# Kernel tuning notes

Hardware: AMD Instinct MI355X
Metric: run time of the kernel (lower is better)

Reference implementation:

```python
import jax, jax.numpy as jnp
import numpy as np

N = 50000
E = 800000
D = 128
LN_EPS = 1e-5


def setup_inputs() -> dict:
    key = jax.random.key(0)
    k1, k2, k3, k4 = jax.random.split(key, 4)
    x = jax.random.normal(k1, (N, D), dtype=jnp.float32)
    edge_index = jax.random.randint(k2, (2, E), 0, N, dtype=jnp.int32)
    # xavier_uniform with gain=sqrt(2) (relu gain)
    gain = float(np.sqrt(2.0))
    lim_lin = gain * float(np.sqrt(6.0 / (D + D)))
    W_lin = jax.random.uniform(k3, (D, D), dtype=jnp.float32, minval=-lim_lin, maxval=lim_lin)
    lim_attn = gain * float(np.sqrt(6.0 / (2 * D + 1)))
    W_attn = jax.random.uniform(k4, (1, 2 * D), dtype=jnp.float32, minval=-lim_attn, maxval=lim_attn)
    ln_scale = jnp.ones((D,), dtype=jnp.float32)
    ln_bias = jnp.zeros((D,), dtype=jnp.float32)
    return {"x": x, "W_lin": W_lin, "W_attn": W_attn,
            "ln_scale": ln_scale, "ln_bias": ln_bias, "edge_index": edge_index}


def _layer_norm(h, scale, bias):
    mu = jnp.mean(h, axis=-1, keepdims=True)
    var = jnp.mean(jnp.square(h - mu), axis=-1, keepdims=True)
    return (h - mu) * jax.lax.rsqrt(var + LN_EPS) * scale + bias


def reference(x, W_lin, W_attn, ln_scale, ln_bias, edge_index):
    n = x.shape[0]
    src, dst = edge_index[0], edge_index[1]
    # h = x @ W_lin^T  [N, D]
    h = jnp.einsum('nd,od->no', x, W_lin)
    # attention score: [h_src || h_dst] @ W_attn^T == h_src@a_src + h_dst@a_dst
    d = h.shape[1]
    a_src = W_attn[0, :d]
    a_dst = W_attn[0, d:]
    s_src = h @ a_src  # [N]
    s_dst = h @ a_dst  # [N]
    scores = s_src[src] + s_dst[dst]  # [E]
    scores = jnp.where(scores >= 0, scores, 0.2 * scores)  # leaky_relu(0.2)
    # segment softmax over edges grouped by dst
    seg_max = jax.ops.segment_max(scores, dst, num_segments=n)  # [N]
    seg_max = jnp.where(jnp.isfinite(seg_max), seg_max, 0.0)
    ex = jnp.exp(scores - seg_max[dst])  # [E]
    denom = jax.ops.segment_sum(ex, dst, num_segments=n)  # [N]
    alpha = ex / jnp.where(denom > 0, denom, 1.0)[dst]  # [E]
    # weighted message aggregation (dropout is identity in eval mode)
    msgs = h[src] * alpha[:, None]  # [E, D]
    agg = jax.ops.segment_sum(msgs, dst, num_segments=n)  # [N, D]
    # residual (input_dim == output_dim -> no projection) + layer norm
    return _layer_norm(agg + x, ln_scale, ln_bias)
```

## Files before the change

kernel.cpp:

```cpp
#include <hip/hip_runtime.h>

#define N_NODES 50000
#define E_EDGES 800000
#define D_DIM   128
#define LN_EPS  1e-5f
#define SCAN_BLOCKS 196
#define HIST_BLOCKS 3125
#define GEMM_BLOCKS 391

typedef __bf16 bf16x8 __attribute__((ext_vector_type(8)));
typedef unsigned short ushort8v __attribute__((ext_vector_type(8)));
typedef float f32x4 __attribute__((ext_vector_type(4)));
typedef int i32x2v __attribute__((ext_vector_type(2)));
typedef int i32x16v __attribute__((ext_vector_type(16)));

__device__ inline unsigned short f2b(float f) {
    unsigned int u = __float_as_uint(f);
    unsigned int r = u + 0x7FFFu + ((u >> 16) & 1u);
    return (unsigned short)(r >> 16);
}
__device__ inline float b2f(unsigned short h) {
    return __uint_as_float((unsigned int)h << 16);
}
__device__ inline float blo(unsigned int u) { return __uint_as_float(u << 16); }
__device__ inline float bhi(unsigned int u) { return __uint_as_float(u & 0xFFFF0000u); }

__device__ inline i32x16v sload16(const uint2* p) {
    i32x16v r;
    asm volatile("s_load_dwordx16 %0, %1, 0x0\n\ts_waitcnt lgkmcnt(0)"
                 : "=&s"(r) : "s"(p));
    return r;
}
__device__ inline i32x2v sload2(const uint2* p) {
    i32x2v r;
    asm volatile("s_load_dwordx2 %0, %1, 0x0\n\ts_waitcnt lgkmcnt(0)"
                 : "=&s"(r) : "s"(p));
    return r;
}

__global__ void k_prep(const float* __restrict__ W,
                       unsigned short* __restrict__ Whp,
                       unsigned short* __restrict__ Wlp,
                       int* __restrict__ count) {
    int i = blockIdx.x * 256 + threadIdx.x;
    if (i < N_NODES) count[i] = 0;
    if (i < 16384) {
        int o = i >> 7, k = i & 127;
        float v = W[i];
        unsigned short h = f2b(v);
        unsigned short l = f2b(v - b2f(h));
        int idx = (k >> 3) * 1024 + o * 8 + (k & 7);
        Whp[idx] = h;
        Wlp[idx] = l;
    }
}

__global__ __launch_bounds__(256, 2) void k_gemm_hist(
        const float* __restrict__ x, const unsigned short* __restrict__ Wpk,
        const float* __restrict__ Wa, const int* __restrict__ dst,
        int* __restrict__ count, unsigned short* __restrict__ hb,
        float* __restrict__ ssrc, float* __restrict__ sdst) {
    __shared__ float4 wl4[4096];
    const int tid = threadIdx.x;

    if (blockIdx.x >= GEMM_BLOCKS) {
        int e = (blockIdx.x - GEMM_BLOCKS) * 256 + tid;
        atomicAdd(&count[dst[e]], 1);
        return;
    }

    {
        const float4* wsrc = (const float4*)Wpk;
        #pragma unroll
        for (int i = 0; i < 16; ++i)
            wl4[i * 256 + tid] = wsrc[i * 256 + tid];
    }

    const int c = tid & 15;
    const int g = (tid >> 4) & 3;
    const int w = tid >> 6;
    const int n0 = blockIdx.x * 128;

    bf16x8 ah[2][4], al[2][4];
    #pragma unroll
    for (int t = 0; t < 2; ++t) {
        int n = n0 + w * 32 + t * 16 + c;
        if (n > N_NODES - 1) n = N_NODES - 1;
        const float* xr = x + (size_t)n * 128;
        #pragma unroll
        for (int s = 0; s < 4; ++s) {
            float4 f0 = *(const float4*)(xr + s * 32 + g * 8);
            float4 f1 = *(const float4*)(xr + s * 32 + g * 8 + 4);
            float fv[8] = {f0.x, f0.y, f0.z, f0.w, f1.x, f1.y, f1.z, f1.w};
            ushort8v uh, ul;
            #pragma unroll
            for (int j = 0; j < 8; ++j) {
                unsigned short hj = f2b(fv[j]);
                uh[j] = hj;
                ul[j] = f2b(fv[j] - b2f(hj));
            }
            ah[t][s] = __builtin_bit_cast(bf16x8, uh);
            al[t][s] = __builtin_bit_cast(bf16x8, ul);
        }
    }

    __syncthreads();
    const bf16x8* wb = (const bf16x8*)wl4;

    f32x4 acc[2][8];
    #pragma unroll
    for (int t = 0; t < 2; ++t)
        #pragma unroll
        for (int cb = 0; cb < 8; ++cb)
            acc[t][cb] = (f32x4){0.f, 0.f, 0.f, 0.f};

    #pragma unroll
    for (int cb = 0; cb < 8; ++cb) {
        #pragma unroll
        for (int s = 0; s < 4; ++s) {
            int q = (s * 4 + g) * 128 + cb * 16 + c;
            bf16x8 bh = wb[q];
            bf16x8 bl = wb[2048 + q];
            acc[0][cb] = __builtin_amdgcn_mfma_f32_16x16x32_bf16(ah[0][s], bh, acc[0][cb], 0, 0, 0);
            acc[1][cb] = __builtin_amdgcn_mfma_f32_16x16x32_bf16(ah[1][s], bh, acc[1][cb], 0, 0, 0);
            acc[0][cb] = __builtin_amdgcn_mfma_f32_16x16x32_bf16(al[0][s], bh, acc[0][cb], 0, 0, 0);
            acc[1][cb] = __builtin_amdgcn_mfma_f32_16x16x32_bf16(al[1][s], bh, acc[1][cb], 0, 0, 0);
            acc[0][cb] = __builtin_amdgcn_mfma_f32_16x16x32_bf16(ah[0][s], bl, acc[0][cb], 0, 0, 0);
            acc[1][cb] = __builtin_amdgcn_mfma_f32_16x16x32_bf16(ah[1][s], bl, acc[1][cb], 0, 0, 0);
        }
    }

    float asv[8], adv[8];
    #pragma unroll
    for (int cb = 0; cb < 8; ++cb) {
        asv[cb] = Wa[cb * 16 + c];
        adv[cb] = Wa[128 + cb * 16 + c];
    }
    #pragma unroll
    for (int t = 0; t < 2; ++t) {
        #pragma unroll
        for (int i = 0; i < 4; ++i) {
            int n = n0 + w * 32 + t * 16 + g * 4 + i;
            float ps = 0.f, pd = 0.f;
            #pragma unroll
            for (int cb = 0; cb < 8; ++cb) {
                float v = acc[t][cb][i];
                ps += v * asv[cb];
                pd += v * adv[cb];
            }
            #pragma unroll
            for (int off = 1; off < 16; off <<= 1) {
                ps += __shfl_xor(ps, off);
                pd += __shfl_xor(pd, off);
            }
            if (n < N_NODES) {
                size_t rb = (size_t)n * 128 + c;
                #pragma unroll
                for (int cb = 0; cb < 8; ++cb)
                    hb[rb + cb * 16] = f2b(acc[t][cb][i]);
                if (c == 0) { ssrc[n] = ps; sdst[n] = pd; }
            }
        }
    }
}

__global__ __launch_bounds__(256) void k_scan1(const int* __restrict__ count,
                                               int* __restrict__ rowptr,
                                               int* __restrict__ bsum) {
    __shared__ int wsum[4];
    const int tid  = threadIdx.x;
    const int lane = tid & 63, w = tid >> 6;
    int i = blockIdx.x * 256 + tid;
    int v = (i < N_NODES) ? count[i] : 0;
    int sc = v;
    #pragma unroll
    for (int off = 1; off < 64; off <<= 1) {
        int t = __shfl_up(sc, off);
        if (lane >= off) sc += t;
    }
    if (lane == 63) wsum[w] = sc;
    __syncthreads();
    if (tid == 0) {
        int s0 = wsum[0], s1 = wsum[1], s2 = wsum[2], s3 = wsum[3];
        wsum[0] = 0; wsum[1] = s0; wsum[2] = s0 + s1; wsum[3] = s0 + s1 + s2;
        bsum[blockIdx.x] = s0 + s1 + s2 + s3;
    }
    __syncthreads();
    if (i < N_NODES) rowptr[i] = sc - v + wsum[w];
}

__global__ __launch_bounds__(256) void k_scan2(int* __restrict__ bsum) {
    __shared__ int wsum[4];
    const int tid  = threadIdx.x;
    const int lane = tid & 63, w = tid >> 6;
    int v = (tid < SCAN_BLOCKS) ? bsum[tid] : 0;
    int sc = v;
    #pragma unroll
    for (int off = 1; off < 64; off <<= 1) {
        int t = __shfl_up(sc, off);
        if (lane >= off) sc += t;
    }
    if (lane == 63) wsum[w] = sc;
    __syncthreads();
    if (tid == 0) {
        int s0 = wsum[0], s1 = wsum[1], s2 = wsum[2];
        wsum[3] = s0 + s1 + s2; wsum[2] = s0 + s1; wsum[1] = s0; wsum[0] = 0;
    }
    __syncthreads();
    if (tid < SCAN_BLOCKS) bsum[tid] = sc - v + wsum[w];
}

__global__ void k_scatter(const int* __restrict__ src, const int* __restrict__ dst,
                          const float* __restrict__ ssrc, const float* __restrict__ sdst,
                          const int* __restrict__ rowptr, const int* __restrict__ bsum,
                          int* __restrict__ count, uint2* __restrict__ sev) {
    int e = blockIdx.x * 256 + threadIdx.x;
    int s  = src[e];
    int dv = dst[e];
    float sc = ssrc[s] + sdst[dv];
    sc = sc >= 0.f ? sc : 0.2f * sc;
    float ex = __expf(sc);
    int pos = rowptr[dv] + bsum[dv >> 8] + (atomicSub(&count[dv], 1) - 1);
    sev[pos] = make_uint2((unsigned int)s, __float_as_uint(ex));
}

__global__ __launch_bounds__(256) void k_gather(
        const int* __restrict__ rowptr, const int* __restrict__ bsum,
        const uint2* __restrict__ sev,
        const unsigned short* __restrict__ hb, const float* __restrict__ x,
        const float* __restrict__ scale, const float* __restrict__ bias,
        float* __restrict__ out) {
    int n    = __builtin_amdgcn_readfirstlane(blockIdx.x * 4 + (threadIdx.x >> 6));
    int lane = threadIdx.x & 63;
    int beg = rowptr[n] + bsum[n >> 8];
    int end = (n == N_NODES - 1) ? E_EDGES : rowptr[n + 1] + bsum[(n + 1) >> 8];
    const unsigned int* hb32 = (const unsigned int*)hb;

    float a0 = 0.f, a1 = 0.f, b0 = 0.f, b1 = 0.f, den = 0.f, den2 = 0.f;

    int i = beg;
    for (; i + 15 < end; i += 16) {
        int ib = __builtin_amdgcn_readfirstlane(i);
        i32x16v s0 = sload16(sev + ib);
        i32x16v s1 = sload16(sev + ib + 8);
        unsigned int u[16];
        #pragma unroll
        for (int q = 0; q < 8; ++q)
            u[q] = hb32[(((unsigned)s0[2 * q]) << 6) + lane];
        #pragma unroll
        for (int q = 0; q < 8; ++q)
            u[8 + q] = hb32[(((unsigned)s1[2 * q]) << 6) + lane];
        #pragma unroll
        for (int q = 0; q < 8; q += 2) {
            float ex0 = __uint_as_float(s0[2 * q + 1]);
            float ex1 = __uint_as_float(s0[2 * q + 3]);
            den  += ex0; den2 += ex1;
            a0 += ex0 * blo(u[q]);     a1 += ex0 * bhi(u[q]);
            b0 += ex1 * blo(u[q + 1]); b1 += ex1 * bhi(u[q + 1]);
        }
        #pragma unroll
        for (int q = 0; q < 8; q += 2) {
            float ex0 = __uint_as_float(s1[2 * q + 1]);
            float ex1 = __uint_as_float(s1[2 * q + 3]);
            den  += ex0; den2 += ex1;
            a0 += ex0 * blo(u[8 + q]);     a1 += ex0 * bhi(u[8 + q]);
            b0 += ex1 * blo(u[8 + q + 1]); b1 += ex1 * bhi(u[8 + q + 1]);
        }
    }
    for (; i + 7 < end; i += 8) {
        int ib = __builtin_amdgcn_readfirstlane(i);
        i32x16v s0 = sload16(sev + ib);
        unsigned int u[8];
        #pragma unroll
        for (int q = 0; q < 8; ++q)
            u[q] = hb32[(((unsigned)s0[2 * q]) << 6) + lane];
        #pragma unroll
        for (int q = 0; q < 8; q += 2) {
            float ex0 = __uint_as_float(s0[2 * q + 1]);
            float ex1 = __uint_as_float(s0[2 * q + 3]);
            den  += ex0; den2 += ex1;
            a0 += ex0 * blo(u[q]);     a1 += ex0 * bhi(u[q]);
            b0 += ex1 * blo(u[q + 1]); b1 += ex1 * bhi(u[q + 1]);
        }
    }
    for (; i < end; ++i) {
        i32x2v p2 = sload2(sev + __builtin_amdgcn_readfirstlane(i));
        unsigned int u0 = hb32[(((unsigned)p2[0]) << 6) + lane];
        float ex0 = __uint_as_float(p2[1]);
        den += ex0;
        a0 += ex0 * blo(u0);
        a1 += ex0 * bhi(u0);
    }
    a0 += b0; a1 += b1; den += den2;

    float inv_d = 1.f / (den > 0.f ? den : 1.f);
    size_t base = (size_t)n * 128 + 2 * lane;
    float2 xv = *(const float2*)&x[base];
    float r0 = a0 * inv_d + xv.x;
    float r1 = a1 * inv_d + xv.y;

    float sum = r0 + r1;
    #pragma unroll
    for (int off = 32; off >= 1; off >>= 1) sum += __shfl_xor(sum, off);
    float mu = sum * (1.f / 128.f);
    float d0 = r0 - mu, d1 = r1 - mu;
    float ss = d0 * d0 + d1 * d1;
    #pragma unroll
    for (int off = 32; off >= 1; off >>= 1) ss += __shfl_xor(ss, off);
    float inv = rsqrtf(ss * (1.f / 128.f) + LN_EPS);
    float o0 = d0 * inv * scale[2 * lane]     + bias[2 * lane];
    float o1 = d1 * inv * scale[2 * lane + 1] + bias[2 * lane + 1];
    *(float2*)&out[base] = make_float2(o0, o1);
}

extern "C" void kernel_launch(void* const* d_in, const int* in_sizes, int n_in,
                              void* d_out, int out_size, void* d_ws, size_t ws_size,
                              hipStream_t stream) {
    const float* x        = (const float*)d_in[0];
    const float* W_lin    = (const float*)d_in[1];
    const float* W_attn   = (const float*)d_in[2];
    const float* ln_scale = (const float*)d_in[3];
    const float* ln_bias  = (const float*)d_in[4];
    const int*   edge     = (const int*)d_in[5];
    const int*   e_src    = edge;
    const int*   e_dst    = edge + E_EDGES;
    float* out = (float*)d_out;

    char* ws = (char*)d_ws;
    unsigned short* hb  = (unsigned short*)(ws);
    unsigned short* Whp = (unsigned short*)(ws + 12800000);
    unsigned short* Wlp = (unsigned short*)(ws + 12832768);
    float* ssrc   = (float*)(ws + 12865536);
    float* sdst   = (float*)(ws + 13065536);
    int*   count  = (int*)  (ws + 13265536);
    int*   rowptr = (int*)  (ws + 13465536);
    int*   bsum   = (int*)  (ws + 13665552);
    uint2* sev    = (uint2*)(ws + 13666352);

    k_prep     <<<SCAN_BLOCKS, 256, 0, stream>>>(W_lin, Whp, Wlp, count);
    k_gemm_hist<<<GEMM_BLOCKS + HIST_BLOCKS, 256, 0, stream>>>(
                    x, Whp, W_attn, e_dst, count, hb, ssrc, sdst);
    k_scan1    <<<SCAN_BLOCKS, 256, 0, stream>>>(count, rowptr, bsum);
    k_scan2    <<<1,    256, 0, stream>>>(bsum);
    k_scatter  <<<HIST_BLOCKS, 256, 0, stream>>>(e_src, e_dst, ssrc, sdst,
                                                 rowptr, bsum, count, sev);
    k_gather   <<<12500, 256, 0, stream>>>(rowptr, bsum, sev, hb, x,
                                           ln_scale, ln_bias, out);
}
```

Baseline: 200.4 us.

## Record per-edge rank in histogram pass, drop scatter atomics, stage bf16 stores via LDS

The histogram pass now keeps the value returned by each atomicAdd as a per-edge rank and writes it to a new erank buffer. The scatter kernel then computes each edge's slot from rowptr, bsum and that rank, so the second round of atomicSub on count is no longer needed. Both edge kernels process four edges per thread with int4 loads. The GEMM epilogue now stages the bf16 h tile in LDS and writes it out as 16-byte rows instead of scattered 2-byte stores. The cost is an extra 3.2 MB erank write and read, plus extra barriers in the GEMM.

```diff
diff --git a/kernel.cpp b/kernel.cpp
--- a/kernel.cpp
+++ b/kernel.cpp
@@ -5,8 +5,9 @@
 #define D_DIM   128
 #define LN_EPS  1e-5f
 #define SCAN_BLOCKS 196
-#define HIST_BLOCKS 3125
 #define GEMM_BLOCKS 391
+#define HIST4_BLOCKS 782
+#define SCAT_BLOCKS  782
 
 typedef __bf16 bf16x8 __attribute__((ext_vector_type(8)));
 typedef unsigned short ushort8v __attribute__((ext_vector_type(8)));
@@ -58,14 +59,22 @@
 __global__ __launch_bounds__(256, 2) void k_gemm_hist(
         const float* __restrict__ x, const unsigned short* __restrict__ Wpk,
         const float* __restrict__ Wa, const int* __restrict__ dst,
-        int* __restrict__ count, unsigned short* __restrict__ hb,
+        int* __restrict__ count, int* __restrict__ erank,
+        unsigned short* __restrict__ hb,
         float* __restrict__ ssrc, float* __restrict__ sdst) {
     __shared__ float4 wl4[4096];
     const int tid = threadIdx.x;
 
     if (blockIdx.x >= GEMM_BLOCKS) {
-        int e = (blockIdx.x - GEMM_BLOCKS) * 256 + tid;
-        atomicAdd(&count[dst[e]], 1);
+        int e0 = (blockIdx.x - GEMM_BLOCKS) * 1024 + tid * 4;
+        if (e0 < E_EDGES) {
+            int4 dv = *(const int4*)&dst[e0];
+            int r0 = atomicAdd(&count[dv.x], 1);
+            int r1 = atomicAdd(&count[dv.y], 1);
+            int r2 = atomicAdd(&count[dv.z], 1);
+            int r3 = atomicAdd(&count[dv.w], 1);
+            *(int4*)&erank[e0] = make_int4(r0, r1, r2, r3);
+        }
         return;
     }
 
@@ -153,13 +162,29 @@
                 ps += __shfl_xor(ps, off);
                 pd += __shfl_xor(pd, off);
             }
-            if (n < N_NODES) {
-                size_t rb = (size_t)n * 128 + c;
-                #pragma unroll
-                for (int cb = 0; cb < 8; ++cb)
-                    hb[rb + cb * 16] = f2b(acc[t][cb][i]);
-                if (c == 0) { ssrc[n] = ps; sdst[n] = pd; }
-            }
+            if (c == 0 && n < N_NODES) { ssrc[n] = ps; sdst[n] = pd; }
+        }
+    }
+
+    __syncthreads();
+    unsigned short* hlds = (unsigned short*)wl4;
+    #pragma unroll
+    for (int t = 0; t < 2; ++t)
+        #pragma unroll
+        for (int cb = 0; cb < 8; ++cb)
+            #pragma unroll
+            for (int i = 0; i < 4; ++i)
+                hlds[(w * 32 + t * 16 + g * 4 + i) * 128 + cb * 16 + c] =
+                    f2b(acc[t][cb][i]);
+    __syncthreads();
+    #pragma unroll
+    for (int ii = 0; ii < 8; ++ii) {
+        int cidx = ii * 256 + tid;
+        int row = cidx >> 4, off = cidx & 15;
+        int n = n0 + row;
+        if (n < N_NODES) {
+            ushort8v v = *(const ushort8v*)&hlds[row * 128 + off * 8];
+            *(ushort8v*)&hb[(size_t)n * 128 + off * 8] = v;
         }
     }
 }
@@ -210,18 +235,31 @@
     if (tid < SCAN_BLOCKS) bsum[tid] = sc - v + wsum[w];
 }
 
-__global__ void k_scatter(const int* __restrict__ src, const int* __restrict__ dst,
-                          const float* __restrict__ ssrc, const float* __restrict__ sdst,
-                          const int* __restrict__ rowptr, const int* __restrict__ bsum,
-                          int* __restrict__ count, uint2* __restrict__ sev) {
-    int e = blockIdx.x * 256 + threadIdx.x;
-    int s  = src[e];
-    int dv = dst[e];
-    float sc = ssrc[s] + sdst[dv];
-    sc = sc >= 0.f ? sc : 0.2f * sc;
-    float ex = __expf(sc);
-    int pos = rowptr[dv] + bsum[dv >> 8] + (atomicSub(&count[dv], 1) - 1);
-    sev[pos] = make_uint2((unsigned int)s, __float_as_uint(ex));
+__global__ __launch_bounds__(256) void k_scatter(
+        const int* __restrict__ src, const int* __restrict__ dst,
+        const int* __restrict__ erank,
+        const float* __restrict__ ssrc, const float* __restrict__ sdst,
+        const int* __restrict__ rowptr, const int* __restrict__ bsum,
+        uint2* __restrict__ sev) {
+    int e0 = (blockIdx.x * 256 + threadIdx.x) * 4;
+    if (e0 >= E_EDGES) return;
+    int4 sv = *(const int4*)&src[e0];
+    int4 dv = *(const int4*)&dst[e0];
+    int4 rk = *(const int4*)&erank[e0];
+    float ss0 = ssrc[sv.x], ss1 = ssrc[sv.y], ss2 = ssrc[sv.z], ss3 = ssrc[sv.w];
+    float sd0 = sdst[dv.x], sd1 = sdst[dv.y], sd2 = sdst[dv.z], sd3 = sdst[dv.w];
+    int rp0 = rowptr[dv.x], rp1 = rowptr[dv.y], rp2 = rowptr[dv.z], rp3 = rowptr[dv.w];
+    int bs0 = bsum[dv.x >> 8], bs1 = bsum[dv.y >> 8];
+    int bs2 = bsum[dv.z >> 8], bs3 = bsum[dv.w >> 8];
+    float c0 = ss0 + sd0, c1 = ss1 + sd1, c2 = ss2 + sd2, c3 = ss3 + sd3;
+    c0 = c0 >= 0.f ? c0 : 0.2f * c0;
+    c1 = c1 >= 0.f ? c1 : 0.2f * c1;
+    c2 = c2 >= 0.f ? c2 : 0.2f * c2;
+    c3 = c3 >= 0.f ? c3 : 0.2f * c3;
+    sev[rp0 + bs0 + rk.x] = make_uint2((unsigned int)sv.x, __float_as_uint(__expf(c0)));
+    sev[rp1 + bs1 + rk.y] = make_uint2((unsigned int)sv.y, __float_as_uint(__expf(c1)));
+    sev[rp2 + bs2 + rk.z] = make_uint2((unsigned int)sv.z, __float_as_uint(__expf(c2)));
+    sev[rp3 + bs3 + rk.w] = make_uint2((unsigned int)sv.w, __float_as_uint(__expf(c3)));
 }
 
 __global__ __launch_bounds__(256) void k_gather(
@@ -336,14 +374,15 @@
     int*   rowptr = (int*)  (ws + 13465536);
     int*   bsum   = (int*)  (ws + 13665552);
     uint2* sev    = (uint2*)(ws + 13666352);
+    int*   erank  = (int*)  (ws + 20066352);
 
     k_prep     <<<SCAN_BLOCKS, 256, 0, stream>>>(W_lin, Whp, Wlp, count);
-    k_gemm_hist<<<GEMM_BLOCKS + HIST_BLOCKS, 256, 0, stream>>>(
-                    x, Whp, W_attn, e_dst, count, hb, ssrc, sdst);
+    k_gemm_hist<<<GEMM_BLOCKS + HIST4_BLOCKS, 256, 0, stream>>>(
+                    x, Whp, W_attn, e_dst, count, erank, hb, ssrc, sdst);
     k_scan1    <<<SCAN_BLOCKS, 256, 0, stream>>>(count, rowptr, bsum);
     k_scan2    <<<1,    256, 0, stream>>>(bsum);
-    k_scatter  <<<HIST_BLOCKS, 256, 0, stream>>>(e_src, e_dst, ssrc, sdst,
-                                                 rowptr, bsum, count, sev);
+    k_scatter  <<<SCAT_BLOCKS, 256, 0, stream>>>(e_src, e_dst, erank, ssrc, sdst,
+                                                 rowptr, bsum, sev);
     k_gather   <<<12500, 256, 0, stream>>>(rowptr, bsum, sev, hb, x,
                                            ln_scale, ln_bias, out);
 }
```

New measurement: 179.5 us. -10.4%, faster.
